# Kernel tuning notes

Hardware: AMD Instinct MI355X
Metric: run time of the kernel (lower is better)

The kernel has to match this reference:

```python
import jax, jax.numpy as jnp
import numpy as np

B, L, D, H, HD = 2, 2048, 768, 12, 64
NEG = -1e9

def _rotate_half(x):
    x1, x2 = jnp.split(x, 2, axis=-1)
    return jnp.concatenate([-x2, x1], axis=-1)

def setup_inputs() -> dict:
    key = jax.random.key(0)
    ks = jax.random.split(key, 8)
    hidden_states = jax.random.normal(ks[0], (B, L, D), dtype=jnp.float32)
    # additive causal mask [B,1,L,L]
    causal = jnp.where(jnp.tril(jnp.ones((L, L), dtype=bool)), 0.0, NEG).astype(jnp.float32)
    attention_mask = jnp.broadcast_to(causal[None, None], (B, 1, L, L))
    # RoPE tables [B, L, HD]
    inv_freq = 1.0 / (10000.0 ** (jnp.arange(0, HD, 2, dtype=jnp.float32) / HD))
    angles = jnp.arange(L, dtype=jnp.float32)[:, None] * inv_freq[None, :]  # [L, HD/2]
    emb = jnp.concatenate([angles, angles], axis=-1)  # [L, HD]
    cos = jnp.broadcast_to(jnp.cos(emb)[None], (B, L, HD))
    sin = jnp.broadcast_to(jnp.sin(emb)[None], (B, L, HD))
    s = 0.02
    Wq = s * jax.random.normal(ks[1], (H * HD, D), dtype=jnp.float32)
    Wk = s * jax.random.normal(ks[2], (H * HD, D), dtype=jnp.float32)
    Wv = s * jax.random.normal(ks[3], (H * HD, D), dtype=jnp.float32)
    Wo = s * jax.random.normal(ks[4], (D, H * HD), dtype=jnp.float32)
    return {"hidden_states": hidden_states, "attention_mask": attention_mask,
            "cos": cos, "sin": sin, "Wq": Wq, "Wk": Wk, "Wv": Wv, "Wo": Wo}

def reference(hidden_states, attention_mask, cos, sin, Wq, Wk, Wv, Wo):
    b, l, _ = hidden_states.shape
    def proj(W):  # silu(x @ W.T) -> [B, H, L, HD]
        y = jax.nn.silu(jnp.einsum('bld,ed->ble', hidden_states, W))
        return y.reshape(b, l, H, HD).transpose(0, 2, 1, 3)
    q, k, v = proj(Wq), proj(Wk), proj(Wv)
    c = cos[:, None]  # [B,1,L,HD]
    s = sin[:, None]
    q = q * c + _rotate_half(q) * s
    k = k * c + _rotate_half(k) * s
    attn = jnp.einsum('bhqd,bhkd->bhqk', q, k)
    attn = attn + attention_mask
    attn = jax.nn.silu(attn) / l
    out = jnp.einsum('bhqk,bhkd->bhqd', attn, v)  # [B,H,L,HD]
    out = out.transpose(0, 2, 1, 3).reshape(b, l, H * HD)
    attn_output = jnp.einsum('ble,de->bld', out, Wo)
    return attn_output, attn
```

## Files before the change

kernel.cpp:

```cpp
#include <hip/hip_runtime.h>
#include <cstddef>

#define Bc   2
#define Lc   2048
#define Dc   768
#define Hc   12
#define HDc  64
#define Mrows (Bc * Lc)
#define PAD  72

typedef _Float16 half8 __attribute__((ext_vector_type(8)));
typedef unsigned short ushort8 __attribute__((ext_vector_type(8)));
typedef __attribute__((ext_vector_type(4))) float floatx4;

__device__ __forceinline__ float silu_f(float x) {
    return x / (1.0f + __expf(-x));
}
__device__ __forceinline__ unsigned short f2h(float x) {
    _Float16 h = (_Float16)x;
    return __builtin_bit_cast(unsigned short, h);
}

__global__ __launch_bounds__(256)
void gemm_qkv(const float* __restrict__ hs,
              const float* __restrict__ Wq, const float* __restrict__ Wk,
              const float* __restrict__ Wv,
              const float* __restrict__ cosb, const float* __restrict__ sinb,
              unsigned short* __restrict__ q16, unsigned short* __restrict__ k16,
              unsigned short* __restrict__ vT16) {
    __shared__ unsigned short Af[64][PAD];
    __shared__ unsigned short Wf[64][PAD];
    const int tid  = threadIdx.x;
    const int lane = tid & 63, w = tid >> 6;
    const int m = lane & 15, quad = lane >> 4;
    const int m0 = blockIdx.y * 64;
    const int nblk = blockIdx.x;
    const int which = nblk / 12;
    const int n0 = (nblk - which * 12) * 64;
    const float* __restrict__ W = (which == 0) ? Wq : (which == 1) ? Wk : Wv;

    floatx4 acc[4] = {{0.f,0.f,0.f,0.f},{0.f,0.f,0.f,0.f},
                      {0.f,0.f,0.f,0.f},{0.f,0.f,0.f,0.f}};

    for (int kc = 0; kc < Dc; kc += 64) {
        __syncthreads();
#pragma unroll
        for (int p = 0; p < 4; ++p) {
            const int f = tid + p * 256;
            const int row = f >> 4, c4 = (f & 15) << 2;
            const float4 ta = *(const float4*)(hs + (size_t)(m0 + row) * Dc + kc + c4);
            *(ushort4*)&Af[row][c4] = make_ushort4(f2h(ta.x), f2h(ta.y), f2h(ta.z), f2h(ta.w));
            const float4 tw = *(const float4*)(W + (size_t)(n0 + row) * Dc + kc + c4);
            *(ushort4*)&Wf[row][c4] = make_ushort4(f2h(tw.x), f2h(tw.y), f2h(tw.z), f2h(tw.w));
        }
        __syncthreads();

        const half8 a0 = *(const half8*)&Af[w * 16 + m][quad * 8];
        const half8 a1 = *(const half8*)&Af[w * 16 + m][32 + quad * 8];
#pragma unroll
        for (int nn = 0; nn < 4; ++nn) {
            const half8 b0 = *(const half8*)&Wf[nn * 16 + m][quad * 8];
            const half8 b1 = *(const half8*)&Wf[nn * 16 + m][32 + quad * 8];
            acc[nn] = __builtin_amdgcn_mfma_f32_16x16x32_f16(a0, b0, acc[nn], 0, 0, 0);
            acc[nn] = __builtin_amdgcn_mfma_f32_16x16x32_f16(a1, b1, acc[nn], 0, 0, 0);
        }
    }

    if (which < 2) {
        unsigned short* __restrict__ dst = which ? k16 : q16;
        const int h = n0 >> 6;
#pragma unroll
        for (int r = 0; r < 4; ++r) {
            const int row = m0 + w * 16 + quad * 4 + r;
            const int b = row >> 11, l = row & (Lc - 1);
            const size_t cb   = ((size_t)b * Lc + l) * HDc;
            const size_t base = ((size_t)(b * Hc + h) * Lc + l) * HDc;
            const float ya = silu_f(acc[0][r]);
            const float yb = silu_f(acc[1][r]);
            const float yc = silu_f(acc[2][r]);
            const float yd = silu_f(acc[3][r]);
            dst[base + m]      = f2h(ya * cosb[cb + m]      - yc * sinb[cb + m]);
            dst[base + m + 16] = f2h(yb * cosb[cb + m + 16] - yd * sinb[cb + m + 16]);
            dst[base + m + 32] = f2h(yc * cosb[cb + m + 32] + ya * sinb[cb + m + 32]);
            dst[base + m + 48] = f2h(yd * cosb[cb + m + 48] + yb * sinb[cb + m + 48]);
        }
    } else {
#pragma unroll
        for (int nn = 0; nn < 4; ++nn) {
            const int col = n0 + nn * 16 + m;
            const int h = col >> 6, hd = col & 63;
            const int row0 = m0 + w * 16 + quad * 4;
            const int b = row0 >> 11, l0 = row0 & (Lc - 1);
            const ushort4 hh = make_ushort4(f2h(silu_f(acc[nn][0])), f2h(silu_f(acc[nn][1])),
                                            f2h(silu_f(acc[nn][2])), f2h(silu_f(acc[nn][3])));
            *(ushort4*)(vT16 + ((size_t)(b * Hc + h) * HDc + hd) * Lc + l0) = hh;
        }
    }
}

__global__ __launch_bounds__(256)
void attn_kernel(const unsigned short* __restrict__ q16,
                 const unsigned short* __restrict__ k16,
                 const unsigned short* __restrict__ vT16,
                 float* __restrict__ attn_out,
                 unsigned short* __restrict__ o16) {
    __shared__ unsigned short Qf[64][PAD];
    __shared__ unsigned short Kf[64][PAD];
    __shared__ unsigned short Vt[64][PAD];
    __shared__ unsigned short Ps[64][PAD];

    const int tid  = threadIdx.x;
    const int lane = tid & 63, w = tid >> 6;
    const int m = lane & 15, quad = lane >> 4;

    const int x = blockIdx.x;
    const int bh = blockIdx.y;
    const int band = bh >> 3;
    int qt;
    if (band == 0)      qt = x;
    else if (band == 1) qt = (x + 16) & 31;
    else                qt = (x < 16) ? (30 - 2 * x) : (63 - 2 * x);

    const int b = bh / Hc, h = bh - b * Hc;
    const size_t qkv = (size_t)bh * Lc * HDc;
    const float invL = 1.0f / (float)Lc;

    const int srow = tid >> 3, sc8 = (tid & 7) << 3;
    const unsigned short* kbase = k16 + qkv;
    const unsigned short* vbase = vT16 + (size_t)bh * HDc * Lc;

    {
        const unsigned short* qp = q16 + qkv + (size_t)(qt * 64) * HDc;
        *(ushort8*)&Qf[srow][sc8]      = *(const ushort8*)(qp + srow * HDc + sc8);
        *(ushort8*)&Qf[srow + 32][sc8] = *(const ushort8*)(qp + (srow + 32) * HDc + sc8);
    }

    ushort8 kreg0, kreg1, vreg0, vreg1;
    kreg0 = *(const ushort8*)(kbase + srow * HDc + sc8);
    kreg1 = *(const ushort8*)(kbase + (srow + 32) * HDc + sc8);
    vreg0 = *(const ushort8*)(vbase + (size_t)srow * Lc + sc8);
    vreg1 = *(const ushort8*)(vbase + (size_t)(srow + 32) * Lc + sc8);
    *(ushort8*)&Kf[srow][sc8]      = kreg0;
    *(ushort8*)&Kf[srow + 32][sc8] = kreg1;
    *(ushort8*)&Vt[srow][sc8]      = vreg0;
    *(ushort8*)&Vt[srow + 32][sc8] = vreg1;
    __syncthreads();

    const half8 bq0 = *(const half8*)&Qf[w * 16 + m][quad * 8];
    const half8 bq1 = *(const half8*)&Qf[w * 16 + m][32 + quad * 8];

    floatx4 oacc[4] = {{0.f,0.f,0.f,0.f},{0.f,0.f,0.f,0.f},
                       {0.f,0.f,0.f,0.f},{0.f,0.f,0.f,0.f}};
    float* attn_base = attn_out + (size_t)bh * Lc * Lc;
    const int gi = qt * 64 + w * 16 + m;

    for (int kt = 0; kt <= qt; ++kt) {
        if (kt < qt) {
            const unsigned short* kp = kbase + (size_t)((kt + 1) * 64) * HDc;
            const unsigned short* vp = vbase + (kt + 1) * 64;
            kreg0 = *(const ushort8*)(kp + srow * HDc + sc8);
            kreg1 = *(const ushort8*)(kp + (srow + 32) * HDc + sc8);
            vreg0 = *(const ushort8*)(vp + (size_t)srow * Lc + sc8);
            vreg1 = *(const ushort8*)(vp + (size_t)(srow + 32) * Lc + sc8);
        }

        const bool diag = (kt == qt);
#pragma unroll
        for (int mm = 0; mm < 4; ++mm) {
            const half8 ak0 = *(const half8*)&Kf[mm * 16 + m][quad * 8];
            const half8 ak1 = *(const half8*)&Kf[mm * 16 + m][32 + quad * 8];
            floatx4 s = {0.f, 0.f, 0.f, 0.f};
            s = __builtin_amdgcn_mfma_f32_16x16x32_f16(ak0, bq0, s, 0, 0, 0);
            s = __builtin_amdgcn_mfma_f32_16x16x32_f16(ak1, bq1, s, 0, 0, 0);
            const int kj0 = mm * 16 + quad * 4;
            const int gj0 = kt * 64 + kj0;
            float v[4];
#pragma unroll
            for (int r = 0; r < 4; ++r) {
                float val = s[r];
                v[r] = (diag && (gj0 + r) > gi) ? 0.0f : silu_f(val) * invL;
            }
            const floatx4 vv = {v[0], v[1], v[2], v[3]};
            __builtin_nontemporal_store(vv, (floatx4*)(attn_base + (size_t)gi * Lc + gj0));
            *(ushort4*)&Ps[w * 16 + m][kj0] = make_ushort4(f2h(v[0]), f2h(v[1]), f2h(v[2]), f2h(v[3]));
        }

        const half8 ap0 = *(const half8*)&Ps[w * 16 + m][quad * 8];
        const half8 ap1 = *(const half8*)&Ps[w * 16 + m][32 + quad * 8];
#pragma unroll
        for (int nn = 0; nn < 4; ++nn) {
            const half8 bv0 = *(const half8*)&Vt[nn * 16 + m][quad * 8];
            const half8 bv1 = *(const half8*)&Vt[nn * 16 + m][32 + quad * 8];
            oacc[nn] = __builtin_amdgcn_mfma_f32_16x16x32_f16(ap0, bv0, oacc[nn], 0, 0, 0);
            oacc[nn] = __builtin_amdgcn_mfma_f32_16x16x32_f16(ap1, bv1, oacc[nn], 0, 0, 0);
        }

        __syncthreads();
        if (kt < qt) {
            *(ushort8*)&Kf[srow][sc8]      = kreg0;
            *(ushort8*)&Kf[srow + 32][sc8] = kreg1;
            *(ushort8*)&Vt[srow][sc8]      = vreg0;
            *(ushort8*)&Vt[srow + 32][sc8] = vreg1;
            __syncthreads();
        }
    }

    {
        const int tx = tid & 15, ty = tid >> 4;
        const floatx4 z = {0.f, 0.f, 0.f, 0.f};
#pragma unroll 1
        for (int kt2 = qt + 1; kt2 < Lc / 64; ++kt2) {
#pragma unroll
            for (int i = 0; i < 4; ++i) {
                const int gi2 = qt * 64 + (ty << 2) + i;
                __builtin_nontemporal_store(z,
                    (floatx4*)(attn_base + (size_t)gi2 * Lc + kt2 * 64 + (tx << 2)));
            }
        }
    }

#pragma unroll
    for (int nn = 0; nn < 4; ++nn)
#pragma unroll
        for (int r = 0; r < 4; ++r) {
            const int gi2 = qt * 64 + w * 16 + quad * 4 + r;
            o16[((size_t)b * Lc + gi2) * Dc + h * HDc + nn * 16 + m] = f2h(oacc[nn][r]);
        }
}

__global__ __launch_bounds__(256)
void gemm_out(const unsigned short* __restrict__ A16, const float* __restrict__ W,
              float* __restrict__ C) {
    __shared__ unsigned short Af[64][PAD];
    __shared__ unsigned short Wf[64][PAD];
    const int tid  = threadIdx.x;
    const int lane = tid & 63, w = tid >> 6;
    const int m = lane & 15, quad = lane >> 4;
    const int m0 = blockIdx.y * 64, n0 = blockIdx.x * 64;

    floatx4 acc[4] = {{0.f,0.f,0.f,0.f},{0.f,0.f,0.f,0.f},
                      {0.f,0.f,0.f,0.f},{0.f,0.f,0.f,0.f}};

    for (int kc = 0; kc < Dc; kc += 64) {
        __syncthreads();
#pragma unroll
        for (int p = 0; p < 2; ++p) {
            const int f = tid + p * 256;
            const int row = f >> 3, c8 = (f & 7) << 3;
            *(ushort8*)&Af[row][c8] = *(const ushort8*)(A16 + (size_t)(m0 + row) * Dc + kc + c8);
        }
#pragma unroll
        for (int p = 0; p < 4; ++p) {
            const int f = tid + p * 256;
            const int row = f >> 4, c4 = (f & 15) << 2;
            const float4 t = *(const float4*)(W + (size_t)(n0 + row) * Dc + kc + c4);
            *(ushort4*)&Wf[row][c4] = make_ushort4(f2h(t.x), f2h(t.y), f2h(t.z), f2h(t.w));
        }
        __syncthreads();

        const half8 a0 = *(const half8*)&Af[w * 16 + m][quad * 8];
        const half8 a1 = *(const half8*)&Af[w * 16 + m][32 + quad * 8];
#pragma unroll
        for (int nn = 0; nn < 4; ++nn) {
            const half8 b0 = *(const half8*)&Wf[nn * 16 + m][quad * 8];
            const half8 b1 = *(const half8*)&Wf[nn * 16 + m][32 + quad * 8];
            acc[nn] = __builtin_amdgcn_mfma_f32_16x16x32_f16(a0, b0, acc[nn], 0, 0, 0);
            acc[nn] = __builtin_amdgcn_mfma_f32_16x16x32_f16(a1, b1, acc[nn], 0, 0, 0);
        }
    }

#pragma unroll
    for (int nn = 0; nn < 4; ++nn) {
        const int col = n0 + nn * 16 + m;
#pragma unroll
        for (int r = 0; r < 4; ++r) {
            const int row = m0 + w * 16 + quad * 4 + r;
            __builtin_nontemporal_store(acc[nn][r], C + (size_t)row * Dc + col);
        }
    }
}

extern "C" void kernel_launch(void* const* d_in, const int* in_sizes, int n_in,
                              void* d_out, int out_size, void* d_ws, size_t ws_size,
                              hipStream_t stream) {
    const float* hs   = (const float*)d_in[0];
    const float* cosb = (const float*)d_in[2];
    const float* sinb = (const float*)d_in[3];
    const float* Wq   = (const float*)d_in[4];
    const float* Wk   = (const float*)d_in[5];
    const float* Wv   = (const float*)d_in[6];
    const float* Wo   = (const float*)d_in[7];

    float* attn_output = (float*)d_out;
    float* attn        = attn_output + (size_t)Mrows * Dc;

    const size_t seg = (size_t)Bc * Hc * Lc * HDc;
    unsigned short* q16  = (unsigned short*)d_ws;
    unsigned short* k16  = q16 + seg;
    unsigned short* vT16 = k16 + seg;
    unsigned short* o16  = vT16 + seg;

    const dim3 blk(256);

    gemm_qkv<<<dim3(36, Mrows / 64), blk, 0, stream>>>(hs, Wq, Wk, Wv, cosb, sinb,
                                                       q16, k16, vT16);
    attn_kernel<<<dim3(Lc / 64, Bc * Hc), blk, 0, stream>>>(q16, k16, vT16, attn, o16);
    gemm_out<<<dim3(Dc / 64, Mrows / 64), blk, 0, stream>>>(o16, Wo, attn_output);
}
```

Before: 586.5 us.

## Enlarge QKV GEMM tiles to 128x128 and stage attn scores through LDS

The QKV projection kernel now computes 128x128 output tiles per block, with each wave owning a 64x64 sub-tile (4x4 MFMA accumulators). This raises operand reuse from shared memory and halves the grid. The attention kernel now writes each score tile to an LDS float buffer, which aliases the Q staging area, and then stores it to global memory row-contiguously. The aim is fully coalesced writes of the large attn output in place of the scattered per-lane 16-byte stores. The costs are more registers in the GEMM, an extra barrier, and an LDS round trip per tile.

Measured after the change: 573.3 us. -2.3%, faster.

```diff
diff --git a/kernel.cpp b/kernel.cpp
--- a/kernel.cpp
+++ b/kernel.cpp
@@ -28,24 +28,24 @@
               const float* __restrict__ cosb, const float* __restrict__ sinb,
               unsigned short* __restrict__ q16, unsigned short* __restrict__ k16,
               unsigned short* __restrict__ vT16) {
-    __shared__ unsigned short Af[64][PAD];
-    __shared__ unsigned short Wf[64][PAD];
+    __shared__ unsigned short Af[128][PAD];
+    __shared__ unsigned short Wf[128][PAD];
     const int tid  = threadIdx.x;
     const int lane = tid & 63, w = tid >> 6;
     const int m = lane & 15, quad = lane >> 4;
-    const int m0 = blockIdx.y * 64;
+    const int wr = w >> 1, wc = w & 1;
+    const int m0 = blockIdx.y * 128;
     const int nblk = blockIdx.x;
-    const int which = nblk / 12;
-    const int n0 = (nblk - which * 12) * 64;
+    const int which = nblk / 6;
+    const int n0 = (nblk - which * 6) * 128;
     const float* __restrict__ W = (which == 0) ? Wq : (which == 1) ? Wk : Wv;
 
-    floatx4 acc[4] = {{0.f,0.f,0.f,0.f},{0.f,0.f,0.f,0.f},
-                      {0.f,0.f,0.f,0.f},{0.f,0.f,0.f,0.f}};
+    floatx4 acc[4][4] = {};
 
     for (int kc = 0; kc < Dc; kc += 64) {
         __syncthreads();
 #pragma unroll
-        for (int p = 0; p < 4; ++p) {
+        for (int p = 0; p < 8; ++p) {
             const int f = tid + p * 256;
             const int row = f >> 4, c4 = (f & 15) << 2;
             const float4 ta = *(const float4*)(hs + (size_t)(m0 + row) * Dc + kc + c4);
@@ -55,30 +55,38 @@
         }
         __syncthreads();
 
-        const half8 a0 = *(const half8*)&Af[w * 16 + m][quad * 8];
-        const half8 a1 = *(const half8*)&Af[w * 16 + m][32 + quad * 8];
-#pragma unroll
-        for (int nn = 0; nn < 4; ++nn) {
-            const half8 b0 = *(const half8*)&Wf[nn * 16 + m][quad * 8];
-            const half8 b1 = *(const half8*)&Wf[nn * 16 + m][32 + quad * 8];
-            acc[nn] = __builtin_amdgcn_mfma_f32_16x16x32_f16(a0, b0, acc[nn], 0, 0, 0);
-            acc[nn] = __builtin_amdgcn_mfma_f32_16x16x32_f16(a1, b1, acc[nn], 0, 0, 0);
+#pragma unroll
+        for (int half = 0; half < 2; ++half) {
+            half8 av[4], bv[4];
+#pragma unroll
+            for (int mi = 0; mi < 4; ++mi)
+                av[mi] = *(const half8*)&Af[wr * 64 + mi * 16 + m][half * 32 + quad * 8];
+#pragma unroll
+            for (int ni = 0; ni < 4; ++ni)
+                bv[ni] = *(const half8*)&Wf[wc * 64 + ni * 16 + m][half * 32 + quad * 8];
+#pragma unroll
+            for (int mi = 0; mi < 4; ++mi)
+#pragma unroll
+                for (int ni = 0; ni < 4; ++ni)
+                    acc[mi][ni] = __builtin_amdgcn_mfma_f32_16x16x32_f16(av[mi], bv[ni], acc[mi][ni], 0, 0, 0);
         }
     }
 
     if (which < 2) {
         unsigned short* __restrict__ dst = which ? k16 : q16;
-        const int h = n0 >> 6;
+        const int h = (n0 >> 6) + wc;
+#pragma unroll
+        for (int mi = 0; mi < 4; ++mi)
 #pragma unroll
         for (int r = 0; r < 4; ++r) {
-            const int row = m0 + w * 16 + quad * 4 + r;
+            const int row = m0 + wr * 64 + mi * 16 + quad * 4 + r;
             const int b = row >> 11, l = row & (Lc - 1);
             const size_t cb   = ((size_t)b * Lc + l) * HDc;
             const size_t base = ((size_t)(b * Hc + h) * Lc + l) * HDc;
-            const float ya = silu_f(acc[0][r]);
-            const float yb = silu_f(acc[1][r]);
-            const float yc = silu_f(acc[2][r]);
-            const float yd = silu_f(acc[3][r]);
+            const float ya = silu_f(acc[mi][0][r]);
+            const float yb = silu_f(acc[mi][1][r]);
+            const float yc = silu_f(acc[mi][2][r]);
+            const float yd = silu_f(acc[mi][3][r]);
             dst[base + m]      = f2h(ya * cosb[cb + m]      - yc * sinb[cb + m]);
             dst[base + m + 16] = f2h(yb * cosb[cb + m + 16] - yd * sinb[cb + m + 16]);
             dst[base + m + 32] = f2h(yc * cosb[cb + m + 32] + ya * sinb[cb + m + 32]);
@@ -86,13 +94,15 @@
         }
     } else {
 #pragma unroll
-        for (int nn = 0; nn < 4; ++nn) {
-            const int col = n0 + nn * 16 + m;
+        for (int mi = 0; mi < 4; ++mi)
+#pragma unroll
+        for (int ni = 0; ni < 4; ++ni) {
+            const int col = n0 + wc * 64 + ni * 16 + m;
             const int h = col >> 6, hd = col & 63;
-            const int row0 = m0 + w * 16 + quad * 4;
+            const int row0 = m0 + wr * 64 + mi * 16 + quad * 4;
             const int b = row0 >> 11, l0 = row0 & (Lc - 1);
-            const ushort4 hh = make_ushort4(f2h(silu_f(acc[nn][0])), f2h(silu_f(acc[nn][1])),
-                                            f2h(silu_f(acc[nn][2])), f2h(silu_f(acc[nn][3])));
+            const ushort4 hh = make_ushort4(f2h(silu_f(acc[mi][ni][0])), f2h(silu_f(acc[mi][ni][1])),
+                                            f2h(silu_f(acc[mi][ni][2])), f2h(silu_f(acc[mi][ni][3])));
             *(ushort4*)(vT16 + ((size_t)(b * Hc + h) * HDc + hd) * Lc + l0) = hh;
         }
     }
@@ -104,10 +114,11 @@
                  const unsigned short* __restrict__ vT16,
                  float* __restrict__ attn_out,
                  unsigned short* __restrict__ o16) {
-    __shared__ unsigned short Qf[64][PAD];
     __shared__ unsigned short Kf[64][PAD];
     __shared__ unsigned short Vt[64][PAD];
     __shared__ unsigned short Ps[64][PAD];
+    __shared__ float Sf[64][68];
+    unsigned short (*Qf)[PAD] = (unsigned short(*)[PAD])&Sf[0][0];
 
     const int tid  = threadIdx.x;
     const int lane = tid & 63, w = tid >> 6;
@@ -148,6 +159,7 @@
 
     const half8 bq0 = *(const half8*)&Qf[w * 16 + m][quad * 8];
     const half8 bq1 = *(const half8*)&Qf[w * 16 + m][32 + quad * 8];
+    __syncthreads();
 
     floatx4 oacc[4] = {{0.f,0.f,0.f,0.f},{0.f,0.f,0.f,0.f},
                        {0.f,0.f,0.f,0.f},{0.f,0.f,0.f,0.f}};
@@ -181,7 +193,7 @@
                 v[r] = (diag && (gj0 + r) > gi) ? 0.0f : silu_f(val) * invL;
             }
             const floatx4 vv = {v[0], v[1], v[2], v[3]};
-            __builtin_nontemporal_store(vv, (floatx4*)(attn_base + (size_t)gi * Lc + gj0));
+            *(floatx4*)&Sf[w * 16 + m][kj0] = vv;
             *(ushort4*)&Ps[w * 16 + m][kj0] = make_ushort4(f2h(v[0]), f2h(v[1]), f2h(v[2]), f2h(v[3]));
         }
 
@@ -196,6 +208,16 @@
         }
 
         __syncthreads();
+
+#pragma unroll
+        for (int p = 0; p < 4; ++p) {
+            const int f = tid + p * 256;
+            const int row = f >> 4, c = (f & 15) << 2;
+            const floatx4 sv = *(const floatx4*)&Sf[row][c];
+            __builtin_nontemporal_store(sv,
+                (floatx4*)(attn_base + (size_t)(qt * 64 + row) * Lc + kt * 64 + c));
+        }
+
         if (kt < qt) {
             *(ushort8*)&Kf[srow][sc8]      = kreg0;
             *(ushort8*)&Kf[srow + 32][sc8] = kreg1;
@@ -302,8 +324,8 @@
 
     const dim3 blk(256);
 
-    gemm_qkv<<<dim3(36, Mrows / 64), blk, 0, stream>>>(hs, Wq, Wk, Wv, cosb, sinb,
-                                                       q16, k16, vT16);
+    gemm_qkv<<<dim3(18, Mrows / 128), blk, 0, stream>>>(hs, Wq, Wk, Wv, cosb, sinb,
+                                                        q16, k16, vT16);
     attn_kernel<<<dim3(Lc / 64, Bc * Hc), blk, 0, stream>>>(q16, k16, vT16, attn, o16);
     gemm_out<<<dim3(Dc / 64, Mrows / 64), blk, 0, stream>>>(o16, Wo, attn_output);
 }
```
